# Kernel tuning notes

Hardware: AMD Instinct MI355X
Metric: run time of the kernel (lower is better)

The kernel has to match this reference:

```python
import jax, jax.numpy as jnp
import numpy as np

B, C, N, M, H, L = 2, 128, 6000, 1500, 4, 3
DH = C // H


def conv1(x, W, b):
    # 1x1 Conv1d == per-position matmul: x [B,Cin,N], W [Cout,Cin], b [Cout]
    return jnp.einsum('oc,bcn->bon', W, x) + b[None, :, None]


def setup_inputs():
    key = jax.random.key(0)
    ks = jax.random.split(key, 16)
    w = lambda k, shape, fan: (jax.random.normal(k, shape, jnp.float32) / np.sqrt(fan)).astype(jnp.float32)
    inp = {
        'xs': jax.random.normal(ks[0], (B, 1, N, 4), jnp.float32),
        'd': jax.random.normal(ks[1], (B, C, N), jnp.float32),
        'feat_piece': jax.random.normal(ks[2], (B, C, M), jnp.float32),
        'logits_in': jax.random.normal(ks[3], (B, N), jnp.float32),
        'Wq': w(ks[4], (L, C, C), C), 'bq': jnp.zeros((L, C), jnp.float32),
        'Wk': w(ks[5], (L, C, C), C), 'bk': jnp.zeros((L, C), jnp.float32),
        'Wv': w(ks[6], (L, C, C), C), 'bv': jnp.zeros((L, C), jnp.float32),
        'Wm': w(ks[7], (L, C, C), C), 'bm': jnp.zeros((L, C), jnp.float32),
        'Wc1': w(ks[8], (L, 2 * C, 2 * C), 2 * C), 'bc1': jnp.zeros((L, 2 * C), jnp.float32),
        'bns': jnp.ones((L, 2 * C), jnp.float32), 'bnsh': jnp.zeros((L, 2 * C), jnp.float32),
        'Wc2': w(ks[9], (L, C, 2 * C), 2 * C), 'bc2': jnp.zeros((L, C), jnp.float32),
        'iW1': w(ks[10], (64, C), C), 'ib1': jnp.zeros((64,), jnp.float32),
        'ibn1s': jnp.ones((64,), jnp.float32), 'ibn1sh': jnp.zeros((64,), jnp.float32),
        'iW2': w(ks[11], (16, 64), 64), 'ib2': jnp.zeros((16,), jnp.float32),
        'ibn2s': jnp.ones((16,), jnp.float32), 'ibn2sh': jnp.zeros((16,), jnp.float32),
        'iW3': w(ks[12], (4, 16), 16), 'ib3': jnp.zeros((4,), jnp.float32),
        'ibn3s': jnp.ones((4,), jnp.float32), 'ibn3sh': jnp.zeros((4,), jnp.float32),
        'iW4': w(ks[13], (1, 4), 4), 'ib4': jnp.zeros((1,), jnp.float32),
    }
    return inp


def _forward(xs, d, feat_piece, logits_in, Wq, bq, Wk, bk, Wv, bv, Wm, bm, Wc1, bc1, bns, bnsh, Wc2, bc2,
             iW1, ib1, ibn1s, ibn1sh, iW2, ib2, ibn2s, ibn2sh, iW3, ib3, ibn3s, ibn3sh, iW4, ib4):
    d_old = d
    # kv_mask = (relu(tanh(logits)) > 0) == (logits > 0)
    mask = logits_in > 0.0

    def attention(x1, x2, kv_mask, i):
        bsz = x1.shape[0]
        q = conv1(x1, Wq[i], bq[i]).reshape(bsz, H, DH, -1)  # [B,H,Dh,Nq]
        k = conv1(x2, Wk[i], bk[i]).reshape(bsz, H, DH, -1)  # [B,H,Dh,Nk]
        v = conv1(x2, Wv[i], bv[i]).reshape(bsz, H, DH, -1)
        QK = jnp.einsum('bhdn,bhdm->bhnm', q, k)
        if kv_mask is not None:
            # masked_fill BEFORE the sqrt(head_dim) scaling, as in the original
            QK = jnp.where(kv_mask[:, None, None, :], QK, jnp.float32(-1e6))
        score = jax.nn.softmax(QK / jnp.float32(np.sqrt(DH)), axis=-1)
        add = jnp.einsum('bhnm,bhdm->bhdn', score, v).reshape(bsz, C, -1)
        add = conv1(add, Wm[i], bm[i])
        h = conv1(jnp.concatenate([x1, add], axis=1), Wc1[i], bc1[i])
        # BatchNorm1d (eval) folded into per-channel scale/shift, then ReLU
        h = jax.nn.relu(h * bns[i][None, :, None] + bnsh[i][None, :, None])
        return x1 + conv1(h, Wc2[i], bc2[i])

    feat = attention(feat_piece, d, mask, 0)   # 'cluster':   feat_piece <- d (masked kv)
    feat = attention(feat, feat, None, 1)      # 'context':   self-attention
    d = attention(d, feat, None, 2)            # 'decluster': d <- feat_piece

    def inst_norm(x, eps=1e-3):
        mu = jnp.mean(x, axis=-1, keepdims=True)
        var = jnp.var(x, axis=-1, keepdims=True)  # biased, matches InstanceNorm1d
        return (x - mu) / jnp.sqrt(var + eps)

    def block(x, W, b, s, sh):
        x = inst_norm(conv1(x, W, b))
        return jax.nn.relu(x * s[None, :, None] + sh[None, :, None])

    x = d - d_old
    x = block(x, iW1, ib1, ibn1s, ibn1sh)
    x = block(x, iW2, ib2, ibn2s, ibn2sh)
    x = block(x, iW3, ib3, ibn3s, ibn3sh)
    logits = conv1(x, iW4, ib4)[:, 0, :]  # squeeze channel dim -> [B,N]
    return d, logits  # e_hat is None (loss=False path)


def reference(xs, d, feat_piece, logits_in, Wq, bq, Wk, bk, Wv, bv, Wm, bm, Wc1, bc1, bns, bnsh, Wc2, bc2,
              iW1, ib1, ibn1s, ibn1sh, iW2, ib2, ibn2s, ibn2sh, iW3, ib3, ibn3s, ibn3sh, iW4, ib4):
    return _forward(xs, d, feat_piece, logits_in, Wq, bq, Wk, bk, Wv, bv, Wm, bm, Wc1, bc1, bns, bnsh, Wc2, bc2,
                    iW1, ib1, ibn1s, ibn1sh, iW2, ib2, ibn2s, ibn2sh, iW3, ib3, ibn3s, ibn3sh, iW4, ib4)
```

## Files before the change

### kernel.cpp

```cpp
#include <hip/hip_runtime.h>
#include <math.h>

#define B_  2
#define C_  128
#define N_  6000
#define M_  1500
#define H_  4
#define DH_ 32

typedef __attribute__((ext_vector_type(8))) short bf16x8;
typedef __attribute__((ext_vector_type(4))) float f32x4;
typedef unsigned short u16;

static __device__ __forceinline__ u16 f2bf(float x) {
    unsigned u = __float_as_uint(x);
    return (u16)((u + 0x7fffu + ((u >> 16) & 1u)) >> 16);
}
#define MFMA(a,b,c) __builtin_amdgcn_mfma_f32_16x16x32_bf16((a),(b),(c),0,0,0)
#define INVS2 (0.17677669529663687f * 1.4426950408889634f)

__global__ __launch_bounds__(256) void prep_kernel(
    const float* __restrict__ Wq, const float* __restrict__ Wk, const float* __restrict__ Wv,
    const float* __restrict__ Wm, const float* __restrict__ Wc1, const float* __restrict__ Wc2,
    const float* __restrict__ iW1,
    u16* __restrict__ wq, u16* __restrict__ wk, u16* __restrict__ wv, u16* __restrict__ wm,
    u16* __restrict__ wc1, u16* __restrict__ wc2, u16* __restrict__ w1,
    float* __restrict__ zstats)
{
    long i = (long)blockIdx.x * 256 + threadIdx.x;
    if (i < 512)    zstats[i] = 0.f;
    if (i < 49152)  { wq[i] = f2bf(Wq[i]); wk[i] = f2bf(Wk[i]);
                      wv[i] = f2bf(Wv[i]); wm[i] = f2bf(Wm[i]); }
    if (i < 196608) wc1[i] = f2bf(Wc1[i]);
    if (i < 98304)  wc2[i] = f2bf(Wc2[i]);
    if (i < 8192)   w1[i]  = f2bf(iW1[i]);
}

__global__ __launch_bounds__(256) void qkv_kernel(
    const float* __restrict__ x1, const float* __restrict__ x2, int Pq, int Pk, int Pkpad,
    const u16* __restrict__ wq, const u16* __restrict__ wk, const u16* __restrict__ wv,
    const float* __restrict__ bq, const float* __restrict__ bk, const float* __restrict__ bv,
    u16* __restrict__ Q16, u16* __restrict__ K16, u16* __restrict__ V16)
{
    __shared__ u16 Xt[64][40];
    const int tid = threadIdx.x;
    const int wid = tid >> 6, lane = tid & 63;
    const int l15 = lane & 15, quad = lane >> 4;
    const int job = blockIdx.y >> 1, ot = blockIdx.y & 1;
    const int b = blockIdx.z;
    const int p0 = blockIdx.x * 64;
    const float* X; const u16* W; const float* bias; int P;
    if (job == 0)      { X = x1; W = wq; bias = bq; P = Pq; }
    else if (job == 1) { X = x2; W = wk; bias = bk; P = Pk; }
    else               { X = x2; W = wv; bias = bv; P = Pk; }
    const int Plim = (job == 0) ? Pq : Pkpad;
    if (p0 < Plim) {
        const long xoff = (long)b * C_ * P;
        const int sp = tid & 63, cg = tid >> 6;
        f32x4 acc[4] = {};
        if (p0 < P) {
            for (int k0 = 0; k0 < 128; k0 += 32) {
                bf16x8 st;
                const int pp = (p0 + sp < P) ? p0 + sp : P - 1;
                #pragma unroll
                for (int j = 0; j < 8; ++j)
                    st[j] = (short)f2bf(X[xoff + (long)(k0 + cg * 8 + j) * P + pp]);
                __syncthreads();
                *(bf16x8*)&Xt[sp][cg * 8] = st;
                __syncthreads();
                const bf16x8 af = *(const bf16x8*)(W + (long)(ot * 64 + wid * 16 + l15) * 128 + k0 + quad * 8);
                #pragma unroll
                for (int pg = 0; pg < 4; ++pg) {
                    const bf16x8 bfr = *(const bf16x8*)&Xt[pg * 16 + l15][quad * 8];
                    acc[pg] = MFMA(af, bfr, acc[pg]);
                }
            }
        }
        #pragma unroll
        for (int pg = 0; pg < 4; ++pg)
            #pragma unroll
            for (int r = 0; r < 4; ++r) {
                const int o = ot * 64 + wid * 16 + quad * 4 + r;
                const int p = p0 + pg * 16 + l15;
                if (p >= Plim) continue;
                if (job == 0) {
                    if (p < Pq)
                        Q16[((long)(b * 4 + (o >> 5)) * Pq + p) * 32 + (o & 31)] =
                            f2bf((acc[pg][r] + bias[o]) * INVS2);
                } else {
                    const u16 v = (p < P) ? f2bf(acc[pg][r] + bias[o]) : (u16)0;
                    if (job == 1)
                        K16[((long)(b * 4 + (o >> 5)) * Pkpad + p) * 32 + (o & 31)] = v;
                    else
                        V16[((long)(b * 4 + (o >> 5)) * 48 + (o & 31)) * Pkpad + p] = v;
                }
            }
        if (job == 2) {
            for (int e = tid; e < 2048; e += 256) {
                const int which = e >> 10;
                const int row = 32 + ((e >> 6) & 15);
                const int col = p0 + (e & 63);
                if (col < Pkpad)
                    V16[((long)(b * 4 + ot * 2 + which) * 48 + row) * Pkpad + col] =
                        (row == 32) ? (u16)0x3F80 : (u16)0;
            }
        }
    }
}

template<bool MASKED>
__global__ __launch_bounds__(256) void attn_partial(
    const u16* __restrict__ Q16, const u16* __restrict__ K16, const u16* __restrict__ V16,
    const float* __restrict__ lgin,
    float* __restrict__ pl, float* __restrict__ pacc,
    int Nq, int Nk, int Nkpad, int KS, int chunkLen, int npad)
{
    __shared__ u16 Ps[4][32][72];
    const int tid  = threadIdx.x;
    const int wave = tid >> 6, lane = tid & 63;
    const int l15  = lane & 15, quad = lane >> 4;
    const int bid  = blockIdx.x;
    const int bh   = bid & 7, rest = bid >> 3;
    const int split = rest % KS, qblk = rest / KS;
    const int b = bh >> 2;
    const int q0w = qblk * 128 + wave * 32;

    const u16* Qb = Q16 + (long)bh * Nq * 32;
    const u16* Kb = K16 + (long)bh * Nkpad * 32;
    const u16* Vb = V16 + (long)(bh * 48) * Nkpad;

    const int qq0 = min(q0w + l15, Nq - 1);
    const int qq1 = min(q0w + 16 + l15, Nq - 1);
    const bf16x8 qa0 = *(const bf16x8*)(Qb + (long)qq0 * 32 + quad * 8);
    const bf16x8 qa1 = *(const bf16x8*)(Qb + (long)qq1 * 32 + quad * 8);

    bf16x8 onesf;
    #pragma unroll
    for (int j = 0; j < 8; ++j) onesf[j] = (short)(l15 == 0 ? 0x3F80 : 0);

    f32x4 o00={0,0,0,0}, o01={0,0,0,0}, o10={0,0,0,0}, o11={0,0,0,0};
    f32x4 ol0={0,0,0,0}, ol1={0,0,0,0};
    const f32x4 z4 = {0,0,0,0};

    const int kbeg = split * chunkLen;
    const int kend = kbeg + chunkLen;

    for (int m0 = kbeg; m0 < kend; m0 += 64) {
        f32x4 sa0[4], sa1[4];
        #pragma unroll
        for (int kg = 0; kg < 4; ++kg) {
            const bf16x8 ka = *(const bf16x8*)(Kb + (long)(m0 + kg * 16 + l15) * 32 + quad * 8);
            sa0[kg] = MFMA(ka, qa0, z4);
            sa1[kg] = MFMA(ka, qa1, z4);
        }
        #pragma unroll
        for (int kg = 0; kg < 4; ++kg) {
            float p0[4], p1[4];
            if (MASKED) {
                const int kbase = m0 + kg * 16 + quad * 4;
                const float4 mv = *(const float4*)&lgin[(long)b * Nk + min(kbase, Nk - 4)];
                const float* mr = (const float*)&mv;
                #pragma unroll
                for (int r = 0; r < 4; ++r) {
                    const bool good = (kbase + r < Nk) && (mr[r] > 0.f);
                    p0[r] = good ? exp2f(sa0[kg][r]) : 0.f;
                    p1[r] = good ? exp2f(sa1[kg][r]) : 0.f;
                }
            } else {
                #pragma unroll
                for (int r = 0; r < 4; ++r) { p0[r] = exp2f(sa0[kg][r]); p1[r] = exp2f(sa1[kg][r]); }
            }
            const unsigned a0 = (__float_as_uint(p0[0]) >> 16) | (__float_as_uint(p0[1]) & 0xffff0000u);
            const unsigned a1 = (__float_as_uint(p0[2]) >> 16) | (__float_as_uint(p0[3]) & 0xffff0000u);
            const unsigned b0 = (__float_as_uint(p1[0]) >> 16) | (__float_as_uint(p1[1]) & 0xffff0000u);
            const unsigned b1 = (__float_as_uint(p1[2]) >> 16) | (__float_as_uint(p1[3]) & 0xffff0000u);
            *(uint2*)&Ps[wave][l15][kg * 16 + quad * 4]      = make_uint2(a0, a1);
            *(uint2*)&Ps[wave][16 + l15][kg * 16 + quad * 4] = make_uint2(b0, b1);
        }
        const bf16x8 pa0lo = *(const bf16x8*)&Ps[wave][l15][quad * 8];
        const bf16x8 pa0hi = *(const bf16x8*)&Ps[wave][l15][32 + quad * 8];
        const bf16x8 pa1lo = *(const bf16x8*)&Ps[wave][16 + l15][quad * 8];
        const bf16x8 pa1hi = *(const bf16x8*)&Ps[wave][16 + l15][32 + quad * 8];
        const u16* vr0 = Vb + (long)l15 * Nkpad + m0;
        const u16* vr1 = Vb + (long)(16 + l15) * Nkpad + m0;
        const bf16x8 v0lo = *(const bf16x8*)(vr0 + quad * 8);
        const bf16x8 v0hi = *(const bf16x8*)(vr0 + 32 + quad * 8);
        const bf16x8 v1lo = *(const bf16x8*)(vr1 + quad * 8);
        const bf16x8 v1hi = *(const bf16x8*)(vr1 + 32 + quad * 8);
        o00 = MFMA(pa0lo, v0lo, o00); o00 = MFMA(pa0hi, v0hi, o00);
        o01 = MFMA(pa0lo, v1lo, o01); o01 = MFMA(pa0hi, v1hi, o01);
        o10 = MFMA(pa1lo, v0lo, o10); o10 = MFMA(pa1hi, v0hi, o10);
        o11 = MFMA(pa1lo, v1lo, o11); o11 = MFMA(pa1hi, v1hi, o11);
        ol0 = MFMA(pa0lo, onesf, ol0); ol0 = MFMA(pa0hi, onesf, ol0);
        ol1 = MFMA(pa1lo, onesf, ol1); ol1 = MFMA(pa1hi, onesf, ol1);
    }

    const long base = (long)bh * KS + split;
    const float fn = (split == KS - 1) ? (float)npad : 0.f;
    if (l15 == 0) {
        #pragma unroll
        for (int r = 0; r < 4; ++r) {
            const int qA = q0w + quad * 4 + r, qB = qA + 16;
            if (qA < Nq) pl[base * Nq + qA] = ol0[r] - fn;
            if (qB < Nq) pl[base * Nq + qB] = ol1[r] - fn;
        }
    }
    #pragma unroll
    for (int r = 0; r < 4; ++r) {
        const int qA = q0w + quad * 4 + r, qB = qA + 16;
        if (qA < Nq) { float* d = &pacc[((long)base * Nq + qA) * 32]; d[l15] = o00[r]; d[16 + l15] = o01[r]; }
        if (qB < Nq) { float* d = &pacc[((long)base * Nq + qB) * 32]; d[l15] = o10[r]; d[16 + l15] = o11[r]; }
    }
}

__global__ __launch_bounds__(256) void epi_kernel(
    const float* __restrict__ pl, const float* __restrict__ pacc, int KS,
    const float* __restrict__ x1,
    const u16* __restrict__ Wm, const float* __restrict__ bm,
    const u16* __restrict__ Wc1, const float* __restrict__ bc1,
    const float* __restrict__ bns, const float* __restrict__ bnsh,
    const u16* __restrict__ Wc2, const float* __restrict__ bc2,
    float* __restrict__ outF, float* __restrict__ outR, int Nq)
{
    __shared__ u16 Xa[32][136];
    __shared__ u16 Xc[32][264];
    __shared__ u16 Xh[32][264];
    const int tid = threadIdx.x;
    const int wid = tid >> 6, lane = tid & 63;
    const int l15 = lane & 15, quad = lane >> 4;
    const int b = blockIdx.y;
    const int p0 = blockIdx.x * 32;

    {
        const int pos = tid & 31, sub = tid >> 5;
        const int pp = (p0 + pos < Nq) ? p0 + pos : Nq - 1;
        const int h = sub >> 1, d0 = (sub & 1) * 16;
        const int bh = b * 4 + h;
        float lg = 0.f, acc[16];
        #pragma unroll
        for (int i = 0; i < 16; ++i) acc[i] = 0.f;
        for (int s = 0; s < KS; ++s) {
            const long base = (long)bh * KS + s;
            lg += pl[base * Nq + pp];
            const float* src = &pacc[(base * Nq + pp) * 32 + d0];
            #pragma unroll
            for (int i = 0; i < 4; ++i) {
                const float4 v = *(const float4*)&src[i * 4];
                acc[i*4+0] += v.x; acc[i*4+1] += v.y; acc[i*4+2] += v.z; acc[i*4+3] += v.w;
            }
        }
        const float inv = 1.f / lg;
        bf16x8 v0, v1;
        #pragma unroll
        for (int i = 0; i < 8; ++i) { v0[i] = (short)f2bf(acc[i] * inv); v1[i] = (short)f2bf(acc[8 + i] * inv); }
        const int c0 = h * 32 + (sub & 1) * 16;
        *(bf16x8*)&Xa[pos][c0] = v0;
        *(bf16x8*)&Xa[pos][c0 + 8] = v1;
        bf16x8 y0, y1;
        #pragma unroll
        for (int j = 0; j < 8; ++j) {
            y0[j] = (short)f2bf(x1[((long)b * 128 + sub * 16 + j) * Nq + pp]);
            y1[j] = (short)f2bf(x1[((long)b * 128 + sub * 16 + 8 + j) * Nq + pp]);
        }
        *(bf16x8*)&Xc[pos][sub * 16] = y0;
        *(bf16x8*)&Xc[pos][sub * 16 + 8] = y1;
    }
    __syncthreads();

    {
        f32x4 am[2][2] = {};
        for (int k0 = 0; k0 < 128; k0 += 32) {
            #pragma unroll
            for (int og = 0; og < 2; ++og) {
                const bf16x8 af = *(const bf16x8*)(Wm + (long)(wid * 32 + og * 16 + l15) * 128 + k0 + quad * 8);
                #pragma unroll
                for (int pg = 0; pg < 2; ++pg) {
                    const bf16x8 bfr = *(const bf16x8*)&Xa[pg * 16 + l15][k0 + quad * 8];
                    am[og][pg] = MFMA(af, bfr, am[og][pg]);
                }
            }
        }
        #pragma unroll
        for (int og = 0; og < 2; ++og)
            #pragma unroll
            for (int pg = 0; pg < 2; ++pg)
                #pragma unroll
                for (int r = 0; r < 4; ++r) {
                    const int o = wid * 32 + og * 16 + quad * 4 + r;
                    Xc[pg * 16 + l15][128 + o] = f2bf(am[og][pg][r] + bm[o]);
                }
    }
    __syncthreads();

    {
        f32x4 a1[4][2] = {};
        for (int k0 = 0; k0 < 256; k0 += 32) {
            #pragma unroll
            for (int og = 0; og < 4; ++og) {
                const bf16x8 af = *(const bf16x8*)(Wc1 + (long)(wid * 64 + og * 16 + l15) * 256 + k0 + quad * 8);
                #pragma unroll
                for (int pg = 0; pg < 2; ++pg) {
                    const bf16x8 bfr = *(const bf16x8*)&Xc[pg * 16 + l15][k0 + quad * 8];
                    a1[og][pg] = MFMA(af, bfr, a1[og][pg]);
                }
            }
        }
        #pragma unroll
        for (int og = 0; og < 4; ++og)
            #pragma unroll
            for (int pg = 0; pg < 2; ++pg)
                #pragma unroll
                for (int r = 0; r < 4; ++r) {
                    const int o = wid * 64 + og * 16 + quad * 4 + r;
                    const float hv = fmaxf((a1[og][pg][r] + bc1[o]) * bns[o] + bnsh[o], 0.f);
                    Xh[pg * 16 + l15][o] = f2bf(hv);
                }
    }
    __syncthreads();

    {
        f32x4 a2[2][2] = {};
        for (int k0 = 0; k0 < 256; k0 += 32) {
            #pragma unroll
            for (int og = 0; og < 2; ++og) {
                const bf16x8 af = *(const bf16x8*)(Wc2 + (long)(wid * 32 + og * 16 + l15) * 256 + k0 + quad * 8);
                #pragma unroll
                for (int pg = 0; pg < 2; ++pg) {
                    const bf16x8 bfr = *(const bf16x8*)&Xh[pg * 16 + l15][k0 + quad * 8];
                    a2[og][pg] = MFMA(af, bfr, a2[og][pg]);
                }
            }
        }
        #pragma unroll
        for (int og = 0; og < 2; ++og)
            #pragma unroll
            for (int pg = 0; pg < 2; ++pg)
                #pragma unroll
                for (int r = 0; r < 4; ++r) {
                    const int o = wid * 32 + og * 16 + quad * 4 + r;
                    const int p = p0 + pg * 16 + l15;
                    if (p < Nq) {
                        const long idx = ((long)b * 128 + o) * Nq + p;
                        const float v = a2[og][pg][r] + bc2[o];
                        outF[idx] = v + x1[idx];
                        if (outR) outR[idx] = v;
                    }
                }
    }
}

__global__ __launch_bounds__(256) void tail1_kernel(
    const float* __restrict__ X, const u16* __restrict__ W, const float* __restrict__ bias,
    float* __restrict__ Y, float* __restrict__ ps, float* __restrict__ pq, int P)
{
    __shared__ u16 Xt[64][40];
    const int tid = threadIdx.x;
    const int wid = tid >> 6, lane = tid & 63;
    const int l15 = lane & 15, quad = lane >> 4;
    const int b = blockIdx.y;
    const int p0 = blockIdx.x * 64;
    const int sp = tid & 63, cg = tid >> 6;
    f32x4 acc[4] = {};
    for (int k0 = 0; k0 < 128; k0 += 32) {
        bf16x8 st;
        {
            const int pp = (p0 + sp < P) ? p0 + sp : P - 1;
            #pragma unroll
            for (int j = 0; j < 8; ++j)
                st[j] = (short)f2bf(X[((long)b * 128 + k0 + cg * 8 + j) * P + pp]);
        }
        __syncthreads();
        *(bf16x8*)&Xt[sp][cg * 8] = st;
        __syncthreads();
        const bf16x8 af = *(const bf16x8*)(W + (long)(wid * 16 + l15) * 128 + k0 + quad * 8);
        #pragma unroll
        for (int pg = 0; pg < 4; ++pg) {
            const bf16x8 bfr = *(const bf16x8*)&Xt[pg * 16 + l15][quad * 8];
            acc[pg] = MFMA(af, bfr, acc[pg]);
        }
    }
    float sums[4] = {}, sq[4] = {};
    #pragma unroll
    for (int pg = 0; pg < 4; ++pg)
        #pragma unroll
        for (int r = 0; r < 4; ++r) {
            const int o = wid * 16 + quad * 4 + r;
            const int p = p0 + pg * 16 + l15;
            if (p < P) {
                const float v = acc[pg][r] + bias[o];
                Y[((long)b * 64 + o) * P + p] = v;
                sums[r] += v; sq[r] += v * v;
            }
        }
    #pragma unroll
    for (int mk = 1; mk < 16; mk <<= 1)
        #pragma unroll
        for (int r = 0; r < 4; ++r) { sums[r] += __shfl_xor(sums[r], mk); sq[r] += __shfl_xor(sq[r], mk); }
    if (l15 == 0)
        #pragma unroll
        for (int r = 0; r < 4; ++r) {
            const int o = wid * 16 + quad * 4 + r;
            atomicAdd(&ps[b * 64 + o], sums[r]);
            atomicAdd(&pq[b * 64 + o], sq[r]);
        }
}

template<int CI, int CO, bool STATS>
__global__ __launch_bounds__(256) void tail_par(
    const float* __restrict__ xraw, const float* __restrict__ ps, const float* __restrict__ pq,
    const float* __restrict__ sc, const float* __restrict__ sh,
    const float* __restrict__ W, const float* __restrict__ bias,
    float* __restrict__ ps2, float* __restrict__ pq2, float* __restrict__ yout, int P)
{
    __shared__ float k1s[CI], k2s[CI], Wl[CO * CI];
    __shared__ float sS[CO], sQ[CO];
    const int tid = threadIdx.x;
    const int b = blockIdx.y;
    const int pos = tid >> 2, g = tid & 3;
    for (int i = tid; i < CO * CI; i += 256) Wl[i] = W[i];
    if (tid < CI) {
        const float S = ps[b * CI + tid], Q2 = pq[b * CI + tid];
        const float mu = S / P, var = Q2 / P - mu * mu;
        const float rs = rsqrtf(var + 1e-3f);
        k1s[tid] = rs * sc[tid];
        k2s[tid] = sh[tid] - mu * rs * sc[tid];
    }
    if (STATS && tid < CO) { sS[tid] = 0.f; sQ[tid] = 0.f; }
    __syncthreads();

    const int p = blockIdx.x * 64 + pos;
    const bool valid = p < P;
    const int pp = valid ? p : P - 1;
    float acc[CO] = {};
    constexpr int CG = CI / 4;
    #pragma unroll
    for (int i = 0; i < CG; ++i) {
        const int c = g * CG + i;
        const float xn = fmaxf(xraw[((long)b * CI + c) * P + pp] * k1s[c] + k2s[c], 0.f);
        #pragma unroll
        for (int o = 0; o < CO; ++o) acc[o] += Wl[o * CI + c] * xn;
    }
    #pragma unroll
    for (int o = 0; o < CO; ++o) {
        acc[o] += __shfl_xor(acc[o], 1);
        acc[o] += __shfl_xor(acc[o], 2);
        acc[o] += bias[o];
    }
    if (valid) {
        if (CO >= 4) {
            constexpr int OG = CO / 4;
            #pragma unroll
            for (int i = 0; i < OG; ++i) {
                const int o = g * OG + i;
                yout[((long)b * CO + o) * P + p] = acc[o];
            }
        } else if (g == 0) {
            yout[(long)b * P + p] = acc[0];
        }
    }
    if (STATS) {
        float sv[CO], qv[CO];
        #pragma unroll
        for (int o = 0; o < CO; ++o) {
            const float v = (g == 0 && valid) ? acc[o] : 0.f;
            sv[o] = v; qv[o] = v * v;
        }
        #pragma unroll
        for (int mk = 1; mk < 64; mk <<= 1)
            #pragma unroll
            for (int o = 0; o < CO; ++o) { sv[o] += __shfl_xor(sv[o], mk); qv[o] += __shfl_xor(qv[o], mk); }
        if ((tid & 63) == 0)
            #pragma unroll
            for (int o = 0; o < CO; ++o) { atomicAdd(&sS[o], sv[o]); atomicAdd(&sQ[o], qv[o]); }
        __syncthreads();
        if (tid < CO) { atomicAdd(&ps2[b * CO + tid], sS[tid]); atomicAdd(&pq2[b * CO + tid], sQ[tid]); }
    }
}

extern "C" void kernel_launch(void* const* d_in, const int* in_sizes, int n_in,
                              void* d_out, int out_size, void* d_ws, size_t ws_size,
                              hipStream_t stream)
{
    const float* dX   = (const float*)d_in[1];
    const float* fpX  = (const float*)d_in[2];
    const float* lgin = (const float*)d_in[3];
    const float* Wq = (const float*)d_in[4];  const float* bq = (const float*)d_in[5];
    const float* Wk = (const float*)d_in[6];  const float* bk = (const float*)d_in[7];
    const float* Wv = (const float*)d_in[8];  const float* bv = (const float*)d_in[9];
    const float* Wm = (const float*)d_in[10]; const float* bm = (const float*)d_in[11];
    const float* Wc1= (const float*)d_in[12]; const float* bc1= (const float*)d_in[13];
    const float* bns= (const float*)d_in[14]; const float* bnsh=(const float*)d_in[15];
    const float* Wc2= (const float*)d_in[16]; const float* bc2= (const float*)d_in[17];
    const float* iW1= (const float*)d_in[18]; const float* ib1= (const float*)d_in[19];
    const float* s1 = (const float*)d_in[20]; const float* h1 = (const float*)d_in[21];
    const float* iW2= (const float*)d_in[22]; const float* ib2= (const float*)d_in[23];
    const float* s2 = (const float*)d_in[24]; const float* h2 = (const float*)d_in[25];
    const float* iW3= (const float*)d_in[26]; const float* ib3= (const float*)d_in[27];
    const float* s3 = (const float*)d_in[28]; const float* h3 = (const float*)d_in[29];
    const float* iW4= (const float*)d_in[30]; const float* ib4= (const float*)d_in[31];

    float* out_d      = (float*)d_out;
    float* out_logits = out_d + (long)B_ * C_ * N_;

    float* f = (float*)d_ws;
    long off = 0;
    auto alloc = [&](long n) { float* p = f + off; off += n; return p; };
    float* featA = alloc(384000);
    float* featB = alloc(384000);
    float* q16f  = alloc(800000);
    float* k16f  = alloc(800000);
    float* v16f  = alloc(1200000);
    float* xb    = alloc(1536000);
    float* x1raw = alloc(768000);
    float* x2raw = alloc(192000);
    float* x3raw = alloc(48000);
    float* plb   = alloc(100000);
    float* pacc  = alloc(3200000);
    float* zst   = alloc(512);
    float* wreg  = alloc(250000);
    (void)ws_size; (void)in_sizes; (void)n_in; (void)out_size;

    float* ps1 = zst;        float* pq1 = zst + 128;
    float* ps2 = zst + 256;  float* pq2 = zst + 288;
    float* ps3 = zst + 320;  float* pq3 = zst + 328;

    u16* wq_h  = (u16*)wreg;
    u16* wk_h  = wq_h + 49152;
    u16* wv_h  = wk_h + 49152;
    u16* wm_h  = wv_h + 49152;
    u16* wc1_h = wm_h + 49152;
    u16* wc2_h = wc1_h + 196608;
    u16* w1_h  = wc2_h + 98304;

    u16* Q16 = (u16*)q16f;
    u16* K16 = (u16*)k16f;
    u16* V16 = (u16*)v16f;

    prep_kernel<<<dim3(768), 256, 0, stream>>>(Wq, Wk, Wv, Wm, Wc1, Wc2, iW1,
                                               wq_h, wk_h, wv_h, wm_h, wc1_h, wc2_h, w1_h, zst);

    auto layer = [&](const float* x1, const float* x2, int Nq, int Nk,
                     const float* maskl, int li, int KS, int chunkLen,
                     float* outF, float* outR) {
        const int Nkpad = KS * chunkLen;
        const int npad  = maskl ? 0 : (Nkpad - Nk);
        qkv_kernel<<<dim3((max(Nq, Nkpad) + 63) / 64, 6, B_), 256, 0, stream>>>(
            x1, x2, Nq, Nk, Nkpad,
            wq_h + (long)li * 16384, wk_h + (long)li * 16384, wv_h + (long)li * 16384,
            bq + li * 128, bk + li * 128, bv + li * 128, Q16, K16, V16);
        const int qblocks = (Nq + 127) / 128;
        if (maskl)
            attn_partial<true><<<dim3(qblocks * KS * 8), 256, 0, stream>>>(
                Q16, K16, V16, maskl, plb, pacc, Nq, Nk, Nkpad, KS, chunkLen, npad);
        else
            attn_partial<false><<<dim3(qblocks * KS * 8), 256, 0, stream>>>(
                Q16, K16, V16, nullptr, plb, pacc, Nq, Nk, Nkpad, KS, chunkLen, npad);
        epi_kernel<<<dim3((Nq + 31) / 32, B_), 256, 0, stream>>>(
            plb, pacc, KS, x1,
            wm_h + (long)li * 16384, bm + li * 128,
            wc1_h + (long)li * 65536, bc1 + li * 256, bns + li * 256, bnsh + li * 256,
            wc2_h + (long)li * 32768, bc2 + li * 128,
            outF, outR, Nq);
    };

    layer(fpX,   dX,    M_, N_, lgin,    0, 8, 768, featA, nullptr);
    layer(featA, featA, M_, M_, nullptr, 1, 8, 192, featB, nullptr);
    layer(dX,    featB, N_, M_, nullptr, 2, 2, 768, out_d, xb);

    tail1_kernel<<<dim3((N_ + 63) / 64, B_), 256, 0, stream>>>(xb, w1_h, ib1, x1raw, ps1, pq1, N_);
    tail_par<64, 16, true><<<dim3((N_ + 63) / 64, B_), 256, 0, stream>>>(
        x1raw, ps1, pq1, s1, h1, iW2, ib2, ps2, pq2, x2raw, N_);
    tail_par<16, 4, true><<<dim3((N_ + 63) / 64, B_), 256, 0, stream>>>(
        x2raw, ps2, pq2, s2, h2, iW3, ib3, ps3, pq3, x3raw, N_);
    tail_par<4, 1, false><<<dim3((N_ + 63) / 64, B_), 256, 0, stream>>>(
        x3raw, ps3, pq3, s3, h3, iW4, ib4, nullptr, nullptr, out_logits, N_);
}
```

Before: 356.8 us.

## Reduce split-K attention partials with atomics instead of per-split buffers

Attention blocks now atomically add their partial numerators and row sums straight into a single per-query buffer, instead of writing per-split slices that the epilogue then sums. Row sums come from a VALU accumulation with shuffles rather than an extra MFMA against a ones vector. The epilogue reads the single buffer and zeroes it for the next layer, and now handles 16 positions per block instead of 32. The aim is to cut partial-buffer traffic and the split reduction loop, at the cost of contention from float atomics, non-deterministic summation order, and less weight reuse per epilogue block.

```diff
diff --git a/kernel.cpp b/kernel.cpp
--- a/kernel.cpp
+++ b/kernel.cpp
@@ -25,7 +25,7 @@
     const float* __restrict__ iW1,
     u16* __restrict__ wq, u16* __restrict__ wk, u16* __restrict__ wv, u16* __restrict__ wm,
     u16* __restrict__ wc1, u16* __restrict__ wc2, u16* __restrict__ w1,
-    float* __restrict__ zstats)
+    float* __restrict__ zstats, float* __restrict__ pz, long pzN)
 {
     long i = (long)blockIdx.x * 256 + threadIdx.x;
     if (i < 512)    zstats[i] = 0.f;
@@ -34,6 +34,7 @@
     if (i < 196608) wc1[i] = f2bf(Wc1[i]);
     if (i < 98304)  wc2[i] = f2bf(Wc2[i]);
     if (i < 8192)   w1[i]  = f2bf(iW1[i]);
+    for (long j = i; j < pzN; j += 768L * 256) pz[j] = 0.f;
 }
 
 __global__ __launch_bounds__(256) void qkv_kernel(
@@ -101,8 +102,7 @@
                 const int row = 32 + ((e >> 6) & 15);
                 const int col = p0 + (e & 63);
                 if (col < Pkpad)
-                    V16[((long)(b * 4 + ot * 2 + which) * 48 + row) * Pkpad + col] =
-                        (row == 32) ? (u16)0x3F80 : (u16)0;
+                    V16[((long)(b * 4 + ot * 2 + which) * 48 + row) * Pkpad + col] = (u16)0;
             }
         }
     }
@@ -113,7 +113,7 @@
     const u16* __restrict__ Q16, const u16* __restrict__ K16, const u16* __restrict__ V16,
     const float* __restrict__ lgin,
     float* __restrict__ pl, float* __restrict__ pacc,
-    int Nq, int Nk, int Nkpad, int KS, int chunkLen, int npad)
+    int Nq, int Nk, int Nkpad, int KS, int chunkLen)
 {
     __shared__ u16 Ps[4][32][72];
     const int tid  = threadIdx.x;
@@ -134,12 +134,8 @@
     const bf16x8 qa0 = *(const bf16x8*)(Qb + (long)qq0 * 32 + quad * 8);
     const bf16x8 qa1 = *(const bf16x8*)(Qb + (long)qq1 * 32 + quad * 8);
 
-    bf16x8 onesf;
-    #pragma unroll
-    for (int j = 0; j < 8; ++j) onesf[j] = (short)(l15 == 0 ? 0x3F80 : 0);
-
     f32x4 o00={0,0,0,0}, o01={0,0,0,0}, o10={0,0,0,0}, o11={0,0,0,0};
-    f32x4 ol0={0,0,0,0}, ol1={0,0,0,0};
+    float lp0 = 0.f, lp1 = 0.f;
     const f32x4 z4 = {0,0,0,0};
 
     const int kbeg = split * chunkLen;
@@ -170,6 +166,8 @@
                 #pragma unroll
                 for (int r = 0; r < 4; ++r) { p0[r] = exp2f(sa0[kg][r]); p1[r] = exp2f(sa1[kg][r]); }
             }
+            lp0 += (p0[0] + p0[1]) + (p0[2] + p0[3]);
+            lp1 += (p1[0] + p1[1]) + (p1[2] + p1[3]);
             const unsigned a0 = (__float_as_uint(p0[0]) >> 16) | (__float_as_uint(p0[1]) & 0xffff0000u);
             const unsigned a1 = (__float_as_uint(p0[2]) >> 16) | (__float_as_uint(p0[3]) & 0xffff0000u);
             const unsigned b0 = (__float_as_uint(p1[0]) >> 16) | (__float_as_uint(p1[1]) & 0xffff0000u);
@@ -191,30 +189,31 @@
         o01 = MFMA(pa0lo, v1lo, o01); o01 = MFMA(pa0hi, v1hi, o01);
         o10 = MFMA(pa1lo, v0lo, o10); o10 = MFMA(pa1hi, v0hi, o10);
         o11 = MFMA(pa1lo, v1lo, o11); o11 = MFMA(pa1hi, v1hi, o11);
-        ol0 = MFMA(pa0lo, onesf, ol0); ol0 = MFMA(pa0hi, onesf, ol0);
-        ol1 = MFMA(pa1lo, onesf, ol1); ol1 = MFMA(pa1hi, onesf, ol1);
-    }
-
-    const long base = (long)bh * KS + split;
-    const float fn = (split == KS - 1) ? (float)npad : 0.f;
-    if (l15 == 0) {
-        #pragma unroll
-        for (int r = 0; r < 4; ++r) {
-            const int qA = q0w + quad * 4 + r, qB = qA + 16;
-            if (qA < Nq) pl[base * Nq + qA] = ol0[r] - fn;
-            if (qB < Nq) pl[base * Nq + qB] = ol1[r] - fn;
-        }
+    }
+
+    lp0 += __shfl_xor(lp0, 16); lp0 += __shfl_xor(lp0, 32);
+    lp1 += __shfl_xor(lp1, 16); lp1 += __shfl_xor(lp1, 32);
+    if (quad == 0) {
+        const int qa = q0w + l15, qb = q0w + 16 + l15;
+        if (qa < Nq) atomicAdd(&pl[(long)bh * Nq + qa], lp0);
+        if (qb < Nq) atomicAdd(&pl[(long)bh * Nq + qb], lp1);
     }
     #pragma unroll
     for (int r = 0; r < 4; ++r) {
         const int qA = q0w + quad * 4 + r, qB = qA + 16;
-        if (qA < Nq) { float* d = &pacc[((long)base * Nq + qA) * 32]; d[l15] = o00[r]; d[16 + l15] = o01[r]; }
-        if (qB < Nq) { float* d = &pacc[((long)base * Nq + qB) * 32]; d[l15] = o10[r]; d[16 + l15] = o11[r]; }
+        if (qA < Nq) {
+            float* d = &pacc[((long)bh * Nq + qA) * 32];
+            atomicAdd(&d[l15], o00[r]); atomicAdd(&d[16 + l15], o01[r]);
+        }
+        if (qB < Nq) {
+            float* d = &pacc[((long)bh * Nq + qB) * 32];
+            atomicAdd(&d[l15], o10[r]); atomicAdd(&d[16 + l15], o11[r]);
+        }
     }
 }
 
 __global__ __launch_bounds__(256) void epi_kernel(
-    const float* __restrict__ pl, const float* __restrict__ pacc, int KS,
+    float* __restrict__ pl, float* __restrict__ pacc, float npadf,
     const float* __restrict__ x1,
     const u16* __restrict__ Wm, const float* __restrict__ bm,
     const u16* __restrict__ Wc1, const float* __restrict__ bc1,
@@ -222,130 +221,110 @@
     const u16* __restrict__ Wc2, const float* __restrict__ bc2,
     float* __restrict__ outF, float* __restrict__ outR, int Nq)
 {
-    __shared__ u16 Xa[32][136];
-    __shared__ u16 Xc[32][264];
-    __shared__ u16 Xh[32][264];
+    __shared__ u16 Xa[16][136];
+    __shared__ u16 Xc[16][264];
+    __shared__ u16 Xh[16][264];
     const int tid = threadIdx.x;
     const int wid = tid >> 6, lane = tid & 63;
     const int l15 = lane & 15, quad = lane >> 4;
     const int b = blockIdx.y;
-    const int p0 = blockIdx.x * 32;
+    const int p0 = blockIdx.x * 16;
 
     {
-        const int pos = tid & 31, sub = tid >> 5;
-        const int pp = (p0 + pos < Nq) ? p0 + pos : Nq - 1;
-        const int h = sub >> 1, d0 = (sub & 1) * 16;
+        const int pos = tid & 15, sub = tid >> 4;
+        const bool own = (p0 + pos < Nq);
+        const int pp = own ? p0 + pos : Nq - 1;
+        const int h = sub >> 2, d0 = (sub & 3) * 8;
         const int bh = b * 4 + h;
-        float lg = 0.f, acc[16];
-        #pragma unroll
-        for (int i = 0; i < 16; ++i) acc[i] = 0.f;
-        for (int s = 0; s < KS; ++s) {
-            const long base = (long)bh * KS + s;
-            lg += pl[base * Nq + pp];
-            const float* src = &pacc[(base * Nq + pp) * 32 + d0];
-            #pragma unroll
-            for (int i = 0; i < 4; ++i) {
-                const float4 v = *(const float4*)&src[i * 4];
-                acc[i*4+0] += v.x; acc[i*4+1] += v.y; acc[i*4+2] += v.z; acc[i*4+3] += v.w;
-            }
+        float* pls = &pl[(long)bh * Nq + pp];
+        const float lg = *pls - npadf;
+        float* src = &pacc[((long)bh * Nq + pp) * 32 + d0];
+        const float4 v0 = *(const float4*)&src[0];
+        const float4 v1 = *(const float4*)&src[4];
+        if (own) {
+            const float4 z = {0.f, 0.f, 0.f, 0.f};
+            *(float4*)&src[0] = z; *(float4*)&src[4] = z;
+            if ((sub & 3) == 0) *pls = 0.f;
         }
         const float inv = 1.f / lg;
-        bf16x8 v0, v1;
-        #pragma unroll
-        for (int i = 0; i < 8; ++i) { v0[i] = (short)f2bf(acc[i] * inv); v1[i] = (short)f2bf(acc[8 + i] * inv); }
-        const int c0 = h * 32 + (sub & 1) * 16;
-        *(bf16x8*)&Xa[pos][c0] = v0;
-        *(bf16x8*)&Xa[pos][c0 + 8] = v1;
-        bf16x8 y0, y1;
-        #pragma unroll
-        for (int j = 0; j < 8; ++j) {
-            y0[j] = (short)f2bf(x1[((long)b * 128 + sub * 16 + j) * Nq + pp]);
-            y1[j] = (short)f2bf(x1[((long)b * 128 + sub * 16 + 8 + j) * Nq + pp]);
-        }
-        *(bf16x8*)&Xc[pos][sub * 16] = y0;
-        *(bf16x8*)&Xc[pos][sub * 16 + 8] = y1;
+        bf16x8 v;
+        v[0] = (short)f2bf(v0.x * inv); v[1] = (short)f2bf(v0.y * inv);
+        v[2] = (short)f2bf(v0.z * inv); v[3] = (short)f2bf(v0.w * inv);
+        v[4] = (short)f2bf(v1.x * inv); v[5] = (short)f2bf(v1.y * inv);
+        v[6] = (short)f2bf(v1.z * inv); v[7] = (short)f2bf(v1.w * inv);
+        *(bf16x8*)&Xa[pos][h * 32 + d0] = v;
+        bf16x8 y;
+        #pragma unroll
+        for (int j = 0; j < 8; ++j)
+            y[j] = (short)f2bf(x1[((long)b * 128 + sub * 8 + j) * Nq + pp]);
+        *(bf16x8*)&Xc[pos][sub * 8] = y;
     }
     __syncthreads();
 
     {
-        f32x4 am[2][2] = {};
+        f32x4 am[2] = {};
         for (int k0 = 0; k0 < 128; k0 += 32) {
             #pragma unroll
             for (int og = 0; og < 2; ++og) {
                 const bf16x8 af = *(const bf16x8*)(Wm + (long)(wid * 32 + og * 16 + l15) * 128 + k0 + quad * 8);
-                #pragma unroll
-                for (int pg = 0; pg < 2; ++pg) {
-                    const bf16x8 bfr = *(const bf16x8*)&Xa[pg * 16 + l15][k0 + quad * 8];
-                    am[og][pg] = MFMA(af, bfr, am[og][pg]);
-                }
+                const bf16x8 bfr = *(const bf16x8*)&Xa[l15][k0 + quad * 8];
+                am[og] = MFMA(af, bfr, am[og]);
             }
         }
         #pragma unroll
         for (int og = 0; og < 2; ++og)
             #pragma unroll
-            for (int pg = 0; pg < 2; ++pg)
-                #pragma unroll
-                for (int r = 0; r < 4; ++r) {
-                    const int o = wid * 32 + og * 16 + quad * 4 + r;
-                    Xc[pg * 16 + l15][128 + o] = f2bf(am[og][pg][r] + bm[o]);
-                }
+            for (int r = 0; r < 4; ++r) {
+                const int o = wid * 32 + og * 16 + quad * 4 + r;
+                Xc[l15][128 + o] = f2bf(am[og][r] + bm[o]);
+            }
     }
     __syncthreads();
 
     {
-        f32x4 a1[4][2] = {};
+        f32x4 a1[4] = {};
         for (int k0 = 0; k0 < 256; k0 += 32) {
             #pragma unroll
             for (int og = 0; og < 4; ++og) {
                 const bf16x8 af = *(const bf16x8*)(Wc1 + (long)(wid * 64 + og * 16 + l15) * 256 + k0 + quad * 8);
-                #pragma unroll
-                for (int pg = 0; pg < 2; ++pg) {
-                    const bf16x8 bfr = *(const bf16x8*)&Xc[pg * 16 + l15][k0 + quad * 8];
-                    a1[og][pg] = MFMA(af, bfr, a1[og][pg]);
-                }
+                const bf16x8 bfr = *(const bf16x8*)&Xc[l15][k0 + quad * 8];
+                a1[og] = MFMA(af, bfr, a1[og]);
             }
         }
         #pragma unroll
         for (int og = 0; og < 4; ++og)
             #pragma unroll
-            for (int pg = 0; pg < 2; ++pg)
-                #pragma unroll
-                for (int r = 0; r < 4; ++r) {
-                    const int o = wid * 64 + og * 16 + quad * 4 + r;
-                    const float hv = fmaxf((a1[og][pg][r] + bc1[o]) * bns[o] + bnsh[o], 0.f);
-                    Xh[pg * 16 + l15][o] = f2bf(hv);
-                }
+            for (int r = 0; r < 4; ++r) {
+                const int o = wid * 64 + og * 16 + quad * 4 + r;
+                const float hv = fmaxf((a1[og][r] + bc1[o]) * bns[o] + bnsh[o], 0.f);
+                Xh[l15][o] = f2bf(hv);
+            }
     }
     __syncthreads();
 
     {
-        f32x4 a2[2][2] = {};
+        f32x4 a2[2] = {};
         for (int k0 = 0; k0 < 256; k0 += 32) {
             #pragma unroll
             for (int og = 0; og < 2; ++og) {
                 const bf16x8 af = *(const bf16x8*)(Wc2 + (long)(wid * 32 + og * 16 + l15) * 256 + k0 + quad * 8);
-                #pragma unroll
-                for (int pg = 0; pg < 2; ++pg) {
-                    const bf16x8 bfr = *(const bf16x8*)&Xh[pg * 16 + l15][k0 + quad * 8];
-                    a2[og][pg] = MFMA(af, bfr, a2[og][pg]);
+                const bf16x8 bfr = *(const bf16x8*)&Xh[l15][k0 + quad * 8];
+                a2[og] = MFMA(af, bfr, a2[og]);
+            }
+        }
+        const int p = p0 + l15;
+        #pragma unroll
+        for (int og = 0; og < 2; ++og)
+            #pragma unroll
+            for (int r = 0; r < 4; ++r) {
+                const int o = wid * 32 + og * 16 + quad * 4 + r;
+                if (p < Nq) {
+                    const long idx = ((long)b * 128 + o) * Nq + p;
+                    const float v = a2[og][r] + bc2[o];
+                    outF[idx] = v + x1[idx];
+                    if (outR) outR[idx] = v;
                 }
             }
-        }
-        #pragma unroll
-        for (int og = 0; og < 2; ++og)
-            #pragma unroll
-            for (int pg = 0; pg < 2; ++pg)
-                #pragma unroll
-                for (int r = 0; r < 4; ++r) {
-                    const int o = wid * 32 + og * 16 + quad * 4 + r;
-                    const int p = p0 + pg * 16 + l15;
-                    if (p < Nq) {
-                        const long idx = ((long)b * 128 + o) * Nq + p;
-                        const float v = a2[og][pg][r] + bc2[o];
-                        outF[idx] = v + x1[idx];
-                        if (outR) outR[idx] = v;
-                    }
-                }
     }
 }
 
@@ -514,8 +493,8 @@
     float* x1raw = alloc(768000);
     float* x2raw = alloc(192000);
     float* x3raw = alloc(48000);
-    float* plb   = alloc(100000);
-    float* pacc  = alloc(3200000);
+    float* pacc  = alloc(1536000);
+    float* plb   = alloc(48000);
     float* zst   = alloc(512);
     float* wreg  = alloc(250000);
     (void)ws_size; (void)in_sizes; (void)n_in; (void)out_size;
@@ -537,13 +516,14 @@
     u16* V16 = (u16*)v16f;
 
     prep_kernel<<<dim3(768), 256, 0, stream>>>(Wq, Wk, Wv, Wm, Wc1, Wc2, iW1,
-                                               wq_h, wk_h, wv_h, wm_h, wc1_h, wc2_h, w1_h, zst);
+                                               wq_h, wk_h, wv_h, wm_h, wc1_h, wc2_h, w1_h,
+                                               zst, pacc, 1536000L + 48000L);
 
     auto layer = [&](const float* x1, const float* x2, int Nq, int Nk,
                      const float* maskl, int li, int KS, int chunkLen,
                      float* outF, float* outR) {
         const int Nkpad = KS * chunkLen;
-        const int npad  = maskl ? 0 : (Nkpad - Nk);
+        const float npadf = maskl ? 0.f : (float)(Nkpad - Nk);
         qkv_kernel<<<dim3((max(Nq, Nkpad) + 63) / 64, 6, B_), 256, 0, stream>>>(
             x1, x2, Nq, Nk, Nkpad,
             wq_h + (long)li * 16384, wk_h + (long)li * 16384, wv_h + (long)li * 16384,
@@ -551,12 +531,12 @@
         const int qblocks = (Nq + 127) / 128;
         if (maskl)
             attn_partial<true><<<dim3(qblocks * KS * 8), 256, 0, stream>>>(
-                Q16, K16, V16, maskl, plb, pacc, Nq, Nk, Nkpad, KS, chunkLen, npad);
+                Q16, K16, V16, maskl, plb, pacc, Nq, Nk, Nkpad, KS, chunkLen);
         else
             attn_partial<false><<<dim3(qblocks * KS * 8), 256, 0, stream>>>(
-                Q16, K16, V16, nullptr, plb, pacc, Nq, Nk, Nkpad, KS, chunkLen, npad);
-        epi_kernel<<<dim3((Nq + 31) / 32, B_), 256, 0, stream>>>(
-            plb, pacc, KS, x1,
+                Q16, K16, V16, nullptr, plb, pacc, Nq, Nk, Nkpad, KS, chunkLen);
+        epi_kernel<<<dim3((Nq + 15) / 16, B_), 256, 0, stream>>>(
+            plb, pacc, npadf, x1,
             wm_h + (long)li * 16384, bm + li * 128,
             wc1_h + (long)li * 65536, bc1 + li * 256, bns + li * 256, bnsh + li * 256,
             wc2_h + (long)li * 32768, bc2 + li * 128,
```

New measurement: 367.1 us. +2.9%, slower.
